# Kernel tuning notes

Hardware: AMD Instinct MI355X
Metric: run time of the kernel (lower is better)

Reference implementation:

```python
import jax, jax.numpy as jnp
import numpy as np

BETA = 0.25

def setup_inputs() -> dict:
    key = jax.random.key(0)
    k1, k2 = jax.random.split(key)
    x = jax.random.normal(k1, (32, 32, 32, 64), dtype=jnp.float32)
    # tf.random_uniform_initializer default: uniform in [-0.05, 0.05]
    embeddings = jax.random.uniform(k2, (64, 1024), dtype=jnp.float32,
                                    minval=-0.05, maxval=0.05)
    return {"x": x, "embeddings": embeddings}

def reference(x, embeddings):
    D, K = embeddings.shape
    flat = x.reshape(-1, D)                                   # [N, D]
    # squared L2 distances to each codebook vector (expanded form)
    sim = flat @ embeddings                                   # [N, K]
    dists = (jnp.sum(flat * flat, axis=1, keepdims=True)
             + jnp.sum(embeddings * embeddings, axis=0)
             - 2.0 * sim)                                     # [N, K]
    idx = jnp.argmin(dists, axis=1)                           # [N]
    quantized = embeddings.T[idx].reshape(x.shape)            # gather == one-hot matmul
    commitment_loss = BETA * jnp.mean((jax.lax.stop_gradient(quantized) - x) ** 2)
    codebook_loss = jnp.mean((quantized - jax.lax.stop_gradient(x)) ** 2)
    loss = commitment_loss + codebook_loss
    out = x + jax.lax.stop_gradient(quantized - x)            # straight-through
    return out, loss
```

## Files before the change

kernel.cpp:

```cpp
#include <hip/hip_runtime.h>
#include <hip/hip_bf16.h>


#define NROWS 32768
#define DDIM  64
#define KCODE 1024
#define NELEM (NROWS * DDIM)
#define MARGIN 4e-3f
#define MAINBLK 256

typedef __attribute__((ext_vector_type(8))) _Float16 f16x8;
typedef __attribute__((ext_vector_type(4))) float f32x4;

static __device__ __forceinline__ unsigned short f2h(float v) {
    _Float16 h = (_Float16)v;
    unsigned short b;
    __builtin_memcpy(&b, &h, 2);
    return b;
}
static __device__ __forceinline__ void gload16(const void* g, void* l) {
    __builtin_amdgcn_global_load_lds(
        (const __attribute__((address_space(1))) void*)g,
        (__attribute__((address_space(3))) void*)l, 16, 0, 0);
}

__global__ void vq_prep(const float* __restrict__ e,
                        float* __restrict__ se,
                        float* __restrict__ eT,
                        unsigned short* __restrict__ ehSw,
                        int* __restrict__ ctrl) {
    __shared__ float tile[64][17];
    const int t = threadIdx.x;
    const int k0 = blockIdx.x * 16;
    if (blockIdx.x == 0 && t < 4) ctrl[t] = 0;
    #pragma unroll
    for (int i = 0; i < 4; ++i) {
        int idx = i * 256 + t;
        int d = idx >> 4, kk = idx & 15;
        tile[d][kk] = e[d * KCODE + k0 + kk];
    }
    __syncthreads();
    if (t < 16) {
        float s = 0.f;
        #pragma unroll
        for (int d = 0; d < 64; ++d) { float v = tile[d][t]; s = fmaf(v, v, s); }
        se[k0 + t] = s;
    }
    const int kk = t >> 4;
    const int dg = (t & 15) * 4;
    const int kg = k0 + kk;
    float v0 = tile[dg + 0][kk], v1 = tile[dg + 1][kk];
    float v2 = tile[dg + 2][kk], v3 = tile[dg + 3][kk];
    *(float4*)&eT[(size_t)kg * 64 + dg] = make_float4(v0, v1, v2, v3);
    const int sw = (((dg >> 3) ^ (kg & 7)) << 3) + (dg & 7);
    *(ushort4*)&ehSw[(size_t)kg * 64 + sw] =
        make_ushort4(f2h(v0), f2h(v1), f2h(v2), f2h(v3));
}

__launch_bounds__(1024)
__global__ void vq_main(const float* __restrict__ x,
                        const float* __restrict__ se,
                        const float* __restrict__ eT,
                        const unsigned short* __restrict__ ehSw,
                        float* __restrict__ out,
                        float* __restrict__ parts) {
    __shared__ unsigned short Beh[KCODE * 64];
    __shared__ float sse[KCODE];
    __shared__ float wsum[8];
    __shared__ float xs[64];
    __shared__ float cb[1024];
    __shared__ int   ci[1024];
    __shared__ float hv1[2][128], hv2[2][128], hv3[2][128];
    __shared__ int   hi1[2][128], hi2[2][128];
    __shared__ int   lightRows[128];
    __shared__ int   lightA[128];
    __shared__ int   lightB[128];
    __shared__ int   heavyRows[128];
    __shared__ int   idxRow[128];
    __shared__ int   sNl, sNh;

    const int t = threadIdx.x;
    const int lane = t & 63;
    const int w = t >> 6;
    const int w8 = w & 7;
    const int half = w >> 3;
    const int quad = lane >> 4, l15 = lane & 15;
    const int rowBase = blockIdx.x * 128 + w8 * 16;

    if (t == 0) { sNl = 0; sNh = 0; }

    {
        const unsigned char* g = (const unsigned char*)ehSw;
        #pragma unroll
        for (int r = 0; r < 8; ++r)
            gload16(g + (size_t)(r * 1024 + t) * 16, &Beh[(r * 1024 + t) * 8]);
        sse[t] = se[t];
    }

    f16x8 ah0, ah1, al0, al1;
    {
        const float4* ap0 = (const float4*)(x + (size_t)(rowBase + l15) * 64 + quad * 8);
        const float4* ap1 = (const float4*)(x + (size_t)(rowBase + l15) * 64 + 32 + quad * 8);
        float4 a0 = ap0[0], a1 = ap0[1], b0 = ap1[0], b1 = ap1[1];
        float av[8] = {a0.x, a0.y, a0.z, a0.w, a1.x, a1.y, a1.z, a1.w};
        float bv[8] = {b0.x, b0.y, b0.z, b0.w, b1.x, b1.y, b1.z, b1.w};
        f16x8 h0, h1, l0, l1;
        #pragma unroll
        for (int j = 0; j < 8; ++j) {
            _Float16 ha = (_Float16)av[j];
            _Float16 hb = (_Float16)bv[j];
            h0[j] = ha;
            h1[j] = hb;
            l0[j] = (_Float16)(av[j] - (float)ha);
            l1[j] = (_Float16)(bv[j] - (float)hb);
        }
        ah0 = h0; ah1 = h1; al0 = l0; al1 = l1;
    }
    __syncthreads();

    float sb[4], sb2[4], sb3[4];
    int   si[4], si2[4];
    #pragma unroll
    for (int r = 0; r < 4; ++r) {
        sb[r] = 3.4e38f; sb2[r] = 3.4e38f; sb3[r] = 3.4e38f;
        si[r] = 0; si2[r] = 0;
    }

    const int slot0 = ((quad ^ (l15 & 7)) << 3);
    const int slot1 = (((quad + 4) ^ (l15 & 7)) << 3);
    const int codeBase = half * 512;

    #pragma unroll 4
    for (int nt = 0; nt < 32; ++nt) {
        const int code = codeBase + nt * 16 + l15;
        f16x8 b0 = *(const f16x8*)&Beh[code * 64 + slot0];
        f16x8 b1 = *(const f16x8*)&Beh[code * 64 + slot1];
        float cse = sse[code];
        f32x4 aA = {0.f, 0.f, 0.f, 0.f}, aB = {0.f, 0.f, 0.f, 0.f};
        aA = __builtin_amdgcn_mfma_f32_16x16x32_f16(ah0, b0, aA, 0, 0, 0);
        aB = __builtin_amdgcn_mfma_f32_16x16x32_f16(ah1, b1, aB, 0, 0, 0);
        aA = __builtin_amdgcn_mfma_f32_16x16x32_f16(al0, b0, aA, 0, 0, 0);
        aB = __builtin_amdgcn_mfma_f32_16x16x32_f16(al1, b1, aB, 0, 0, 0);
        #pragma unroll
        for (int r = 0; r < 4; ++r) {
            float key = fmaf(-2.f, aA[r] + aB[r], cse);
            bool lt1 = key < sb[r];
            bool lt2 = key < sb2[r];
            bool lt3 = key < sb3[r];
            sb3[r] = lt2 ? sb2[r] : (lt3 ? key : sb3[r]);
            float nsb2 = lt1 ? sb[r] : (lt2 ? key : sb2[r]);
            int   nsi2 = lt1 ? si[r] : (lt2 ? code : si2[r]);
            sb[r]  = lt1 ? key  : sb[r];
            si[r]  = lt1 ? code : si[r];
            sb2[r] = nsb2;
            si2[r] = nsi2;
        }
    }

    #pragma unroll
    for (int m = 1; m < 16; m <<= 1) {
        #pragma unroll
        for (int r = 0; r < 4; ++r) {
            float b1 = __shfl_xor(sb[r],  m, 64);
            int   i1 = __shfl_xor(si[r],  m, 64);
            float b2 = __shfl_xor(sb2[r], m, 64);
            int   i2 = __shfl_xor(si2[r], m, 64);
            float b3 = __shfl_xor(sb3[r], m, 64);
            bool t1 = (b1 < sb[r]) || (b1 == sb[r] && i1 < si[r]);
            float w1 = t1 ? b1 : sb[r];    int wi1 = t1 ? i1 : si[r];
            float l1 = t1 ? sb[r] : b1;    int li1 = t1 ? si[r] : i1;
            float c2 = t1 ? b2 : sb2[r];   int ci2 = t1 ? i2 : si2[r];
            float c3 = t1 ? b3 : sb3[r];
            float o2 = t1 ? sb2[r] : b2;
            bool t2 = (c2 < l1) || (c2 == l1 && ci2 < li1);
            float w2 = t2 ? c2 : l1;       int wi2 = t2 ? ci2 : li1;
            float w3 = t2 ? fminf(l1, c3) : fminf(c2, o2);
            sb[r] = w1; si[r] = wi1; sb2[r] = w2; si2[r] = wi2; sb3[r] = w3;
        }
    }

    if (l15 == 0) {
        #pragma unroll
        for (int r = 0; r < 4; ++r) {
            const int rloc = w8 * 16 + quad * 4 + r;
            hv1[half][rloc] = sb[r];  hi1[half][rloc] = si[r];
            hv2[half][rloc] = sb2[r]; hi2[half][rloc] = si2[r];
            hv3[half][rloc] = sb3[r];
        }
    }
    __syncthreads();

    if (t < 128) {
        float a1 = hv1[0][t]; int ai1 = hi1[0][t];
        float a2 = hv2[0][t]; int ai2 = hi2[0][t];
        float a3 = hv3[0][t];
        float b1 = hv1[1][t]; int bi1 = hi1[1][t];
        float b2 = hv2[1][t]; int bi2 = hi2[1][t];
        float b3 = hv3[1][t];
        bool t1 = (b1 < a1) || (b1 == a1 && bi1 < ai1);
        float w1 = t1 ? b1 : a1;   int wi1 = t1 ? bi1 : ai1;
        float l1 = t1 ? a1 : b1;   int li1 = t1 ? ai1 : bi1;
        float c2 = t1 ? b2 : a2;   int ci2 = t1 ? bi2 : ai2;
        float c3 = t1 ? b3 : a3;
        float o2 = t1 ? a2 : b2;
        bool t2 = (c2 < l1) || (c2 == l1 && ci2 < li1);
        float w2 = t2 ? c2 : l1;   int wi2 = t2 ? ci2 : li1;
        float w3 = t2 ? fminf(l1, c3) : fminf(c2, o2);

        idxRow[t] = wi1;
        if (w2 - w1 < MARGIN) {
            if (w3 - w1 < MARGIN) {
                int p = atomicAdd(&sNh, 1);
                heavyRows[p] = t;
            } else {
                int p = atomicAdd(&sNl, 1);
                lightRows[p] = t;
                lightA[p] = wi1;
                lightB[p] = wi2;
            }
        }
    }
    __syncthreads();

    const int nl = sNl;
    const int nh = sNh;
    if (t < 2 * nl) {
        const int j = t >> 1, s = t & 1;
        const int rloc = lightRows[j];
        const int code = s ? lightB[j] : lightA[j];
        const float4* xr = (const float4*)(x + ((size_t)blockIdx.x * 128 + rloc) * 64);
        const float4* er = (const float4*)(eT + (size_t)code * 64);
        float sx = 0.f, dot = 0.f;
        #pragma unroll
        for (int i4 = 0; i4 < 16; ++i4) {
            float4 xv = xr[i4];
            float4 ev = er[i4];
            sx = fmaf(xv.x, xv.x, sx); sx = fmaf(xv.y, xv.y, sx);
            sx = fmaf(xv.z, xv.z, sx); sx = fmaf(xv.w, xv.w, sx);
            dot = fmaf(xv.x, ev.x, dot); dot = fmaf(xv.y, ev.y, dot);
            dot = fmaf(xv.z, ev.z, dot); dot = fmaf(xv.w, ev.w, dot);
        }
        float dd = (sx + sse[code]) - 2.0f * dot;
        float ddo = __shfl_xor(dd, 1, 64);
        int   ido = __shfl_xor(code, 1, 64);
        bool take = (ddo < dd) || (ddo == dd && ido < code);
        int best = take ? ido : code;
        if (s == 0) idxRow[rloc] = best;
    }

    for (int i = 0; i < nh; ++i) {
        const int rloc = heavyRows[i];
        const size_t grow = (size_t)blockIdx.x * 128 + rloc;
        if (t < 64) xs[t] = x[grow * 64 + t];
        __syncthreads();

        float sx = 0.f;
        #pragma unroll
        for (int d = 0; d < 64; ++d) sx = fmaf(xs[d], xs[d], sx);

        const float4* e0 = (const float4*)(eT + (size_t)t * 64);
        float dot0 = 0.f;
        #pragma unroll
        for (int i4 = 0; i4 < 16; ++i4) {
            float4 v0 = e0[i4];
            float xa = xs[4 * i4 + 0], xb = xs[4 * i4 + 1];
            float xc = xs[4 * i4 + 2], xd = xs[4 * i4 + 3];
            dot0 = fmaf(xa, v0.x, dot0); dot0 = fmaf(xb, v0.y, dot0);
            dot0 = fmaf(xc, v0.z, dot0); dot0 = fmaf(xd, v0.w, dot0);
        }
        float dd0 = (sx + sse[t]) - 2.0f * dot0;
        cb[t] = dd0; ci[t] = t;
        __syncthreads();

        if (t < 64) {
            float B = cb[t]; int I = ci[t];
            #pragma unroll
            for (int s = 64; s < 1024; s += 64) {
                float b = cb[t + s]; int i2 = ci[t + s];
                bool take = (b < B) || (b == B && i2 < I);
                B = take ? b : B;
                I = take ? i2 : I;
            }
            #pragma unroll
            for (int m = 1; m < 64; m <<= 1) {
                float ob = __shfl_xor(B, m, 64);
                int   oi = __shfl_xor(I, m, 64);
                bool take = (ob < B) || (ob == B && oi < I);
                B = take ? ob : B;
                I = take ? oi : I;
            }
            if (t == 0) idxRow[rloc] = I;
        }
        __syncthreads();
    }
    __syncthreads();

    if (w < 8) {
        const int myidx = idxRow[w * 16 + l15];
        const float4* qrow = (const float4*)(eT + (size_t)myidx * 64 + quad * 16);
        const float4* xrow = (const float4*)(x + (size_t)(rowBase + l15) * 64 + quad * 16);
        float4* orow = (float4*)(out + (size_t)(rowBase + l15) * 64 + quad * 16);
        float lsum = 0.f;
        #pragma unroll
        for (int i = 0; i < 4; ++i) {
            float4 q = qrow[i];
            float4 xv = xrow[i];
            float4 o;
            float dx;
            dx = q.x - xv.x; o.x = xv.x + dx; lsum = fmaf(dx, dx, lsum);
            dx = q.y - xv.y; o.y = xv.y + dx; lsum = fmaf(dx, dx, lsum);
            dx = q.z - xv.z; o.z = xv.z + dx; lsum = fmaf(dx, dx, lsum);
            dx = q.w - xv.w; o.w = xv.w + dx; lsum = fmaf(dx, dx, lsum);
            orow[i] = o;
        }
        #pragma unroll
        for (int off = 32; off > 0; off >>= 1)
            lsum += __shfl_down(lsum, off, 64);
        if (lane == 0) wsum[w] = lsum;
    }
    __syncthreads();

    if (t == 0) {
        float s = 0.f;
        #pragma unroll
        for (int i = 0; i < 8; ++i) s += wsum[i];
        parts[blockIdx.x] = s;
    }
}

__launch_bounds__(256)
__global__ void vq_loss(const float* __restrict__ parts,
                        float* __restrict__ out) {
    __shared__ float cb[256];
    const int t = threadIdx.x;
    cb[t] = parts[t];
    __syncthreads();
    if (t < 64) {
        float v = cb[t] + cb[t + 64] + cb[t + 128] + cb[t + 192];
        #pragma unroll
        for (int off = 32; off > 0; off >>= 1)
            v += __shfl_down(v, off, 64);
        if (t == 0) {
            float m = v / (float)NELEM;
            out[NELEM] = 0.25f * m + m;
        }
    }
}

extern "C" void kernel_launch(void* const* d_in, const int* in_sizes, int n_in,
                              void* d_out, int out_size, void* d_ws, size_t ws_size,
                              hipStream_t stream) {
    const float* x = (const float*)d_in[0];
    const float* e = (const float*)d_in[1];
    float* out = (float*)d_out;
    float* ws  = (float*)d_ws;

    float* se            = ws + 64;
    float* eT            = ws + 1280;
    unsigned short* ehSw = (unsigned short*)(ws + 66816);
    float* parts         = ws + 165120;

    vq_prep<<<64, 256, 0, stream>>>(e, se, eT, ehSw, (int*)ws);
    vq_main<<<MAINBLK, 1024, 0, stream>>>(x, se, eT, ehSw, out, parts);
    vq_loss<<<1, 256, 0, stream>>>(parts, out);
}
```

Before: 101.4 us.

## Pack distance key and code index into one uint for top-3 tracking

```diff
diff --git a/kernel.cpp b/kernel.cpp
--- a/kernel.cpp
+++ b/kernel.cpp
@@ -66,6 +66,7 @@
                         float* __restrict__ parts) {
     __shared__ unsigned short Beh[KCODE * 64];
     __shared__ float sse[KCODE];
+    __shared__ float sse32[KCODE];
     __shared__ float wsum[8];
     __shared__ float xs[64];
     __shared__ float cb[1024];
@@ -94,7 +95,9 @@
         #pragma unroll
         for (int r = 0; r < 8; ++r)
             gload16(g + (size_t)(r * 1024 + t) * 16, &Beh[(r * 1024 + t) * 8]);
-        sse[t] = se[t];
+        float s = se[t];
+        sse[t] = s;
+        sse32[t] = s + 32.0f;
     }
 
     f16x8 ah0, ah1, al0, al1;
@@ -118,43 +121,47 @@
     }
     __syncthreads();
 
-    float sb[4], sb2[4], sb3[4];
-    int   si[4], si2[4];
+    unsigned pk1[4], pk2[4], pk3[4];
     #pragma unroll
-    for (int r = 0; r < 4; ++r) {
-        sb[r] = 3.4e38f; sb2[r] = 3.4e38f; sb3[r] = 3.4e38f;
-        si[r] = 0; si2[r] = 0;
-    }
+    for (int r = 0; r < 4; ++r) { pk1[r] = 0xFFFFFFFFu; pk2[r] = 0xFFFFFFFFu; pk3[r] = 0xFFFFFFFFu; }
 
     const int slot0 = ((quad ^ (l15 & 7)) << 3);
     const int slot1 = (((quad + 4) ^ (l15 & 7)) << 3);
     const int codeBase = half * 512;
+    const int base_l = codeBase + l15;
 
     #pragma unroll 4
     for (int nt = 0; nt < 32; ++nt) {
         const int code = codeBase + nt * 16 + l15;
         f16x8 b0 = *(const f16x8*)&Beh[code * 64 + slot0];
         f16x8 b1 = *(const f16x8*)&Beh[code * 64 + slot1];
-        float cse = sse[code];
-        f32x4 aA = {0.f, 0.f, 0.f, 0.f}, aB = {0.f, 0.f, 0.f, 0.f};
+        float cse32 = sse32[code];
+        f32x4 aA = {0.f, 0.f, 0.f, 0.f};
         aA = __builtin_amdgcn_mfma_f32_16x16x32_f16(ah0, b0, aA, 0, 0, 0);
-        aB = __builtin_amdgcn_mfma_f32_16x16x32_f16(ah1, b1, aB, 0, 0, 0);
+        aA = __builtin_amdgcn_mfma_f32_16x16x32_f16(ah1, b1, aA, 0, 0, 0);
         aA = __builtin_amdgcn_mfma_f32_16x16x32_f16(al0, b0, aA, 0, 0, 0);
-        aB = __builtin_amdgcn_mfma_f32_16x16x32_f16(al1, b1, aB, 0, 0, 0);
+        aA = __builtin_amdgcn_mfma_f32_16x16x32_f16(al1, b1, aA, 0, 0, 0);
         #pragma unroll
         for (int r = 0; r < 4; ++r) {
-            float key = fmaf(-2.f, aA[r] + aB[r], cse);
-            bool lt1 = key < sb[r];
-            bool lt2 = key < sb2[r];
-            bool lt3 = key < sb3[r];
-            sb3[r] = lt2 ? sb2[r] : (lt3 ? key : sb3[r]);
-            float nsb2 = lt1 ? sb[r] : (lt2 ? key : sb2[r]);
-            int   nsi2 = lt1 ? si[r] : (lt2 ? code : si2[r]);
-            sb[r]  = lt1 ? key  : sb[r];
-            si[r]  = lt1 ? code : si[r];
-            sb2[r] = nsb2;
-            si2[r] = nsi2;
-        }
+            float key = fmaf(-2.f, aA[r], cse32);
+            unsigned p = (__float_as_uint(key) & 0xFFFFFFE0u) | (unsigned)nt;
+            unsigned h1 = max(p, pk1[r]);
+            pk1[r]      = min(p, pk1[r]);
+            unsigned h2 = max(h1, pk2[r]);
+            pk2[r]      = min(h1, pk2[r]);
+            pk3[r]      = min(h2, pk3[r]);
+        }
+    }
+
+    float sb[4], sb2[4], sb3[4];
+    int   si[4], si2[4];
+    #pragma unroll
+    for (int r = 0; r < 4; ++r) {
+        sb[r]  = __uint_as_float(pk1[r] & 0xFFFFFFE0u);
+        si[r]  = (int)((pk1[r] & 31u) << 4) + base_l;
+        sb2[r] = __uint_as_float(pk2[r] & 0xFFFFFFE0u);
+        si2[r] = (int)((pk2[r] & 31u) << 4) + base_l;
+        sb3[r] = __uint_as_float(pk3[r] & 0xFFFFFFE0u);
     }
 
     #pragma unroll
```

Measured after the change: 97.78 us, median of 2. 1.04x faster.
